# Kernel tuning notes

Measured on AMD Instinct MI355X. Metric: run time of the kernel, lower is better.

## Reference

```python
import jax, jax.numpy as jnp
import numpy as np

# VQ codebook lookup from PhraseModel.vq():
#   dist = ||z[:, None, :] - codebook[None, :, :]||_2  over last axis
#   k = argmin(dist, axis=-1); out = codebook[k]
# We compute squared distances via the expansion ||z||^2 - 2 z.c + ||c||^2
# to avoid materializing the [B, K, D] broadcast difference; argmin over
# squared distance equals argmin over distance, so the output is identical.

B, K, D = 262144, 128, 510

def setup_inputs() -> dict:
    key = jax.random.key(0)
    kz, kc = jax.random.split(key)
    z = jax.random.normal(kz, (B, D), dtype=jnp.float32)
    codebook = jax.random.normal(kc, (K, D), dtype=jnp.float32)
    return {"z": z, "codebook": codebook}

def reference(z, codebook):
    # squared L2 distances, [B, K]
    z_sq = jnp.sum(z * z, axis=-1, keepdims=True)            # [B, 1]
    c_sq = jnp.sum(codebook * codebook, axis=-1)             # [K]
    cross = jnp.einsum('bd,kd->bk', z, codebook)             # [B, K]
    dist2 = z_sq - 2.0 * cross + c_sq[None, :]
    k = jnp.argmin(dist2, axis=-1)                           # [B]
    return codebook[k]                                       # [B, D] gather
```

## Files before the change

kernel.cpp:

```cpp
#include <hip/hip_runtime.h>
#include <hip/hip_bf16.h>

#define NB 262144
#define ZD 510
#define NK 128
#define GAP_THR 0.08f
#define CHUNK 64
#define NCHUNK 8

typedef __attribute__((ext_vector_type(8))) short short8;
typedef __attribute__((ext_vector_type(16))) float f32x16;

__device__ inline void split2(float2 v, uint& hp, uint& lp) {
    __hip_bfloat16 hx = __float2bfloat16(v.x);
    __hip_bfloat16 hy = __float2bfloat16(v.y);
    float rx = v.x - __bfloat162float(hx);
    float ry = v.y - __bfloat162float(hy);
    __hip_bfloat16 lx = __float2bfloat16(rx);
    __hip_bfloat16 ly = __float2bfloat16(ry);
    hp = (uint)__bfloat16_as_ushort(hx) | ((uint)__bfloat16_as_ushort(hy) << 16);
    lp = (uint)__bfloat16_as_ushort(lx) | ((uint)__bfloat16_as_ushort(ly) << 16);
}

__global__ void csq_kernel(const float* __restrict__ cb, float* __restrict__ csq) {
    int k = blockIdx.x, lane = threadIdx.x;
    const float* row = cb + (size_t)k * ZD;
    double s = 0.0;
#pragma unroll
    for (int j = 0; j < 8; ++j) {
        int d = (j << 6) + lane;
        if (d < ZD) { double v = (double)row[d]; s = fma(v, v, s); }
    }
#pragma unroll
    for (int m = 1; m <= 32; m <<= 1) s += __shfl_xor(s, m, 64);
    if (lane == 0) csq[k] = (float)s;
}

__global__ __launch_bounds__(256, 3) void vq_fused(
    const float* __restrict__ z, const float* __restrict__ cb,
    const float* __restrict__ csq, int* __restrict__ kf, float* __restrict__ out) {
    __shared__ __align__(16) ushort cbh[NK * CHUNK];
    __shared__ __align__(16) ushort cbl[NK * CHUNK];
    __shared__ int km[128];

    const int tid   = threadIdx.x;
    const int lane  = tid & 63;
    const int wv    = tid >> 6;
    const int cmod  = lane & 31;
    const int hi    = lane >> 5;
    const int brow0 = blockIdx.x << 7;
    const int wrow0 = brow0 + (wv << 5);

    f32x16 acc[4];
#pragma unroll
    for (int cf = 0; cf < 4; ++cf)
#pragma unroll
        for (int e = 0; e < 16; ++e) acc[cf][e] = 0.f;

    const float* zrow = z + (size_t)(wrow0 + cmod) * ZD;

    for (int c = 0; c < NCHUNK; ++c) {
        const int c0 = c * CHUNK;
        __syncthreads();
#pragma unroll 4
        for (int i = 0; i < 16; ++i) {
            int idx  = tid + (i << 8);
            int code = idx >> 5;
            int dl   = (idx & 31) << 1;
            int dg   = c0 + dl;
            float2 v = (dg < 509) ? *(const float2*)(cb + (size_t)code * ZD + dg)
                                  : make_float2(0.f, 0.f);
            uint hp, lp; split2(v, hp, lp);
            int wa = code * CHUNK + (((dl >> 3) ^ (code & 7)) << 3) + (dl & 7);
            *(uint*)&cbh[wa] = hp;
            *(uint*)&cbl[wa] = lp;
        }
        __syncthreads();

#pragma unroll
        for (int t = 0; t < 4; ++t) {
            const int dbase = c0 + (t << 4) + (hi << 3);
            float2 v0 = *(const float2*)(zrow + dbase);
            float2 v1 = *(const float2*)(zrow + dbase + 2);
            float2 v2 = *(const float2*)(zrow + dbase + 4);
            float2 v3 = (dbase + 6 < ZD) ? *(const float2*)(zrow + dbase + 6)
                                         : make_float2(0.f, 0.f);
            union { uint u[4]; short8 v8; } ah, al;
            split2(v0, ah.u[0], al.u[0]);
            split2(v1, ah.u[1], al.u[1]);
            split2(v2, ah.u[2], al.u[2]);
            split2(v3, ah.u[3], al.u[3]);

            const int sc = (t << 1) | hi;
            const int ba = cmod * CHUNK + ((sc ^ (cmod & 7)) << 3);
#pragma unroll
            for (int cf = 0; cf < 4; ++cf) {
                short8 bh = *(const short8*)&cbh[(cf << 11) + ba];
                short8 bl = *(const short8*)&cbl[(cf << 11) + ba];
                acc[cf] = __builtin_amdgcn_mfma_f32_32x32x16_bf16(al.v8, bh, acc[cf], 0, 0, 0);
                acc[cf] = __builtin_amdgcn_mfma_f32_32x32x16_bf16(ah.v8, bl, acc[cf], 0, 0, 0);
                acc[cf] = __builtin_amdgcn_mfma_f32_32x32x16_bf16(ah.v8, bh, acc[cf], 0, 0, 0);
            }
        }
    }

    float cq[4];
#pragma unroll
    for (int cf = 0; cf < 4; ++cf) cq[cf] = csq[cf * 32 + cmod];

#pragma unroll
    for (int reg = 0; reg < 16; ++reg) {
        float bv = fmaf(-2.f, acc[0][reg], cq[0]);
        int   bk = cmod;
        float m2 = 1e30f;
#pragma unroll
        for (int cf = 1; cf < 4; ++cf) {
            float v = fmaf(-2.f, acc[cf][reg], cq[cf]);
            int  kk = cf * 32 + cmod;
            if (v < bv)      { m2 = bv; bv = v; bk = kk; }
            else if (v < m2) { m2 = v; }
        }
#pragma unroll
        for (int m = 1; m <= 16; m <<= 1) {
            float ov  = __shfl_xor(bv, m, 64);
            int   ok  = __shfl_xor(bk, m, 64);
            float om2 = __shfl_xor(m2, m, 64);
            float nm2 = fminf(fmaxf(bv, ov), fminf(m2, om2));
            bool take = (ov < bv) || (ov == bv && ok < bk);
            bv = take ? ov : bv;
            bk = take ? ok : bk;
            m2 = nm2;
        }
        if (cmod == 0) {
            int rloc = (reg & 3) + ((reg >> 2) << 3) + (hi << 2);
            int enc  = bk;
            if (m2 - bv < GAP_THR) enc |= (int)0x80000000;
            km[(wv << 5) + rloc] = enc;
            kf[wrow0 + rloc] = enc;
        }
    }
    __syncthreads();

    const int half = tid >> 7, h = tid & 127;
    for (int rp = 0; rp < 64; ++rp) {
        int row = (rp << 1) + half;
        int k   = km[row] & 127;
        const float2* src = (const float2*)(cb + (size_t)k * ZD);
        float2*       dst = (float2*)(out + (size_t)(brow0 + row) * ZD);
        dst[h] = src[h];
        if (h < 127) dst[128 + h] = src[128 + h];
    }
}

__global__ __launch_bounds__(256) void repair(
    const float* __restrict__ z, const float* __restrict__ cb,
    const float* __restrict__ csq, const int* __restrict__ kf,
    float* __restrict__ out) {
    __shared__ float zs[512];
    __shared__ int   kmrow[128];
    __shared__ float wm[2];
    __shared__ int   wk[2];
    __shared__ int   kwin;
    const int tid  = threadIdx.x;
    const int row0 = blockIdx.x << 7;
    if (tid < 128) kmrow[tid] = kf[row0 + tid];
    __syncthreads();

    for (int rl = 0; rl < 128; ++rl) {
        if (kmrow[rl] >= 0) continue;
        int row = row0 + rl;
        for (int j = tid; j < 512; j += 256) zs[j] = (j < ZD) ? z[(size_t)row * ZD + j] : 0.f;
        __syncthreads();
        float sc = 1e30f;
        if (tid < NK) {
            const float* cr = cb + (size_t)tid * ZD;
            float s = 0.f;
#pragma unroll 6
            for (int d = 0; d < ZD; ++d) s = fmaf(zs[d], cr[d], s);
            sc = fmaf(-2.f, s, csq[tid]);
        }
        if (tid < 128) {
            float bv = sc; int bk = tid;
#pragma unroll
            for (int m = 1; m <= 32; m <<= 1) {
                float ov = __shfl_xor(bv, m, 64);
                int   ok = __shfl_xor(bk, m, 64);
                bool take = (ov < bv) || (ov == bv && ok < bk);
                bv = take ? ov : bv;
                bk = take ? ok : bk;
            }
            if ((tid & 63) == 0) { wm[tid >> 6] = bv; wk[tid >> 6] = bk; }
        }
        __syncthreads();
        if (tid == 0) {
            bool t1 = (wm[1] < wm[0]) || (wm[1] == wm[0] && wk[1] < wk[0]);
            kwin = t1 ? wk[1] : wk[0];
        }
        __syncthreads();
        int k = kwin;
        const float2* src = (const float2*)(cb + (size_t)k * ZD);
        float2*       dst = (float2*)(out + (size_t)row * ZD);
        if (tid < 255) dst[tid] = src[tid];
        __syncthreads();
    }
}

extern "C" void kernel_launch(void* const* d_in, const int* in_sizes, int n_in,
                              void* d_out, int out_size, void* d_ws, size_t ws_size,
                              hipStream_t stream) {
    const float* z  = (const float*)d_in[0];
    const float* cb = (const float*)d_in[1];
    float* out = (float*)d_out;
    float* csq = (float*)d_ws;
    int*   kf  = (int*)((char*)d_ws + 1024);

    csq_kernel<<<NK, 64, 0, stream>>>(cb, csq);
    vq_fused<<<NB / 128, 256, 0, stream>>>(z, cb, csq, kf, out);
    repair<<<NB / 128, 256, 0, stream>>>(z, cb, csq, kf, out);
}
```

Baseline: 445.2 us.

## Switch VQ distance GEMM to single fp16 MFMA with pre-swizzled codebook and double buffering

```diff
diff --git a/kernel.cpp b/kernel.cpp
--- a/kernel.cpp
+++ b/kernel.cpp
@@ -4,43 +4,50 @@
 #define NB 262144
 #define ZD 510
 #define NK 128
-#define GAP_THR 0.08f
+#define GAP_THR 1.0f
 #define CHUNK 64
 #define NCHUNK 8
 
-typedef __attribute__((ext_vector_type(8))) short short8;
+typedef _Float16 half8 __attribute__((ext_vector_type(8)));
 typedef __attribute__((ext_vector_type(16))) float f32x16;
 
-__device__ inline void split2(float2 v, uint& hp, uint& lp) {
-    __hip_bfloat16 hx = __float2bfloat16(v.x);
-    __hip_bfloat16 hy = __float2bfloat16(v.y);
-    float rx = v.x - __bfloat162float(hx);
-    float ry = v.y - __bfloat162float(hy);
-    __hip_bfloat16 lx = __float2bfloat16(rx);
-    __hip_bfloat16 ly = __float2bfloat16(ry);
-    hp = (uint)__bfloat16_as_ushort(hx) | ((uint)__bfloat16_as_ushort(hy) << 16);
-    lp = (uint)__bfloat16_as_ushort(lx) | ((uint)__bfloat16_as_ushort(ly) << 16);
-}
-
-__global__ void csq_kernel(const float* __restrict__ cb, float* __restrict__ csq) {
-    int k = blockIdx.x, lane = threadIdx.x;
-    const float* row = cb + (size_t)k * ZD;
+#define WS_CB16_OFF 4096
+#define WS_KF_OFF   139264
+
+__global__ void prep_kernel(const float* __restrict__ cb, float* __restrict__ csq,
+                            ushort* __restrict__ cb16) {
+    const int code = blockIdx.x;
+    const int tid  = threadIdx.x;
+    const float* row = cb + (size_t)code * ZD;
+
+    __shared__ double ws_red[4];
     double s = 0.0;
-#pragma unroll
-    for (int j = 0; j < 8; ++j) {
-        int d = (j << 6) + lane;
+    for (int j = 0; j < 2; ++j) {
+        int d = tid + (j << 8);
         if (d < ZD) { double v = (double)row[d]; s = fma(v, v, s); }
     }
 #pragma unroll
     for (int m = 1; m <= 32; m <<= 1) s += __shfl_xor(s, m, 64);
-    if (lane == 0) csq[k] = (float)s;
+    if ((tid & 63) == 0) ws_red[tid >> 6] = s;
+    __syncthreads();
+    if (tid == 0) csq[code] = (float)(ws_red[0] + ws_red[1] + ws_red[2] + ws_red[3]);
+
+    const int sw = code & 7;
+#pragma unroll
+    for (int u = 0; u < 2; ++u) {
+        int o = tid + (u << 8);
+        int c = o >> 6, j = (o >> 3) & 7, e = o & 7;
+        int src_d = (c << 6) | ((j ^ sw) << 3) | e;
+        float v = (src_d < ZD) ? row[src_d] : 0.f;
+        cb16[(c << 13) + (code << 6) + ((o & 63))] = (ushort)__builtin_bit_cast(short, (_Float16)v);
+    }
 }
 
 __global__ __launch_bounds__(256, 3) void vq_fused(
     const float* __restrict__ z, const float* __restrict__ cb,
-    const float* __restrict__ csq, int* __restrict__ kf, float* __restrict__ out) {
-    __shared__ __align__(16) ushort cbh[NK * CHUNK];
-    __shared__ __align__(16) ushort cbl[NK * CHUNK];
+    const uint4* __restrict__ cb16, const float* __restrict__ csq,
+    int* __restrict__ kf, float* __restrict__ out) {
+    __shared__ __align__(16) ushort buf[2][NK * CHUNK];
     __shared__ int km[128];
 
     const int tid   = threadIdx.x;
@@ -59,48 +66,56 @@
 
     const float* zrow = z + (size_t)(wrow0 + cmod) * ZD;
 
+    {
+        uint4 st[4];
+#pragma unroll
+        for (int i = 0; i < 4; ++i) st[i] = cb16[i * 256 + tid];
+#pragma unroll
+        for (int i = 0; i < 4; ++i) ((uint4*)buf[0])[i * 256 + tid] = st[i];
+    }
+    int cur = 0;
+
     for (int c = 0; c < NCHUNK; ++c) {
+        uint4 nxt[4];
+        if (c < NCHUNK - 1) {
+#pragma unroll
+            for (int i = 0; i < 4; ++i) nxt[i] = cb16[(c + 1) * 1024 + i * 256 + tid];
+        }
+        __syncthreads();
+
         const int c0 = c * CHUNK;
-        __syncthreads();
-#pragma unroll 4
-        for (int i = 0; i < 16; ++i) {
-            int idx  = tid + (i << 8);
-            int code = idx >> 5;
-            int dl   = (idx & 31) << 1;
-            int dg   = c0 + dl;
-            float2 v = (dg < 509) ? *(const float2*)(cb + (size_t)code * ZD + dg)
-                                  : make_float2(0.f, 0.f);
-            uint hp, lp; split2(v, hp, lp);
-            int wa = code * CHUNK + (((dl >> 3) ^ (code & 7)) << 3) + (dl & 7);
-            *(uint*)&cbh[wa] = hp;
-            *(uint*)&cbl[wa] = lp;
-        }
-        __syncthreads();
-
+        float2 zr2[16];
 #pragma unroll
         for (int t = 0; t < 4; ++t) {
             const int dbase = c0 + (t << 4) + (hi << 3);
-            float2 v0 = *(const float2*)(zrow + dbase);
-            float2 v1 = *(const float2*)(zrow + dbase + 2);
-            float2 v2 = *(const float2*)(zrow + dbase + 4);
-            float2 v3 = (dbase + 6 < ZD) ? *(const float2*)(zrow + dbase + 6)
-                                         : make_float2(0.f, 0.f);
-            union { uint u[4]; short8 v8; } ah, al;
-            split2(v0, ah.u[0], al.u[0]);
-            split2(v1, ah.u[1], al.u[1]);
-            split2(v2, ah.u[2], al.u[2]);
-            split2(v3, ah.u[3], al.u[3]);
+            zr2[t * 4 + 0] = *(const float2*)(zrow + dbase);
+            zr2[t * 4 + 1] = *(const float2*)(zrow + dbase + 2);
+            zr2[t * 4 + 2] = *(const float2*)(zrow + dbase + 4);
+            zr2[t * 4 + 3] = (dbase + 6 < ZD) ? *(const float2*)(zrow + dbase + 6)
+                                              : make_float2(0.f, 0.f);
+        }
+
+#pragma unroll
+        for (int t = 0; t < 4; ++t) {
+            half8 a;
+            a[0] = (_Float16)zr2[t * 4 + 0].x; a[1] = (_Float16)zr2[t * 4 + 0].y;
+            a[2] = (_Float16)zr2[t * 4 + 1].x; a[3] = (_Float16)zr2[t * 4 + 1].y;
+            a[4] = (_Float16)zr2[t * 4 + 2].x; a[5] = (_Float16)zr2[t * 4 + 2].y;
+            a[6] = (_Float16)zr2[t * 4 + 3].x; a[7] = (_Float16)zr2[t * 4 + 3].y;
 
             const int sc = (t << 1) | hi;
             const int ba = cmod * CHUNK + ((sc ^ (cmod & 7)) << 3);
 #pragma unroll
             for (int cf = 0; cf < 4; ++cf) {
-                short8 bh = *(const short8*)&cbh[(cf << 11) + ba];
-                short8 bl = *(const short8*)&cbl[(cf << 11) + ba];
-                acc[cf] = __builtin_amdgcn_mfma_f32_32x32x16_bf16(al.v8, bh, acc[cf], 0, 0, 0);
-                acc[cf] = __builtin_amdgcn_mfma_f32_32x32x16_bf16(ah.v8, bl, acc[cf], 0, 0, 0);
-                acc[cf] = __builtin_amdgcn_mfma_f32_32x32x16_bf16(ah.v8, bh, acc[cf], 0, 0, 0);
+                half8 b = *(const half8*)&buf[cur][(cf << 11) + ba];
+                acc[cf] = __builtin_amdgcn_mfma_f32_32x32x16_f16(a, b, acc[cf], 0, 0, 0);
             }
+        }
+
+        if (c < NCHUNK - 1) {
+#pragma unroll
+            for (int i = 0; i < 4; ++i) ((uint4*)buf[cur ^ 1])[i * 256 + tid] = nxt[i];
+            cur ^= 1;
         }
     }
 
@@ -165,6 +180,8 @@
     const int row0 = blockIdx.x << 7;
     if (tid < 128) kmrow[tid] = kf[row0 + tid];
     __syncthreads();
+    int nflag = __syncthreads_count(tid < 128 && kmrow[tid] < 0);
+    if (nflag == 0) return;
 
     for (int rl = 0; rl < 128; ++rl) {
         if (kmrow[rl] >= 0) continue;
@@ -210,11 +227,12 @@
                               hipStream_t stream) {
     const float* z  = (const float*)d_in[0];
     const float* cb = (const float*)d_in[1];
-    float* out = (float*)d_out;
-    float* csq = (float*)d_ws;
-    int*   kf  = (int*)((char*)d_ws + 1024);
-
-    csq_kernel<<<NK, 64, 0, stream>>>(cb, csq);
-    vq_fused<<<NB / 128, 256, 0, stream>>>(z, cb, csq, kf, out);
+    float*  out  = (float*)d_out;
+    float*  csq  = (float*)d_ws;
+    ushort* cb16 = (ushort*)((char*)d_ws + WS_CB16_OFF);
+    int*    kf   = (int*)((char*)d_ws + WS_KF_OFF);
+
+    prep_kernel<<<NK, 256, 0, stream>>>(cb, csq, cb16);
+    vq_fused<<<NB / 128, 256, 0, stream>>>(z, cb, (const uint4*)cb16, csq, kf, out);
     repair<<<NB / 128, 256, 0, stream>>>(z, cb, csq, kf, out);
 }
```

Result: slower. 904.5 us (+103.2%).
